# Optimization experiments

Measured on AMD Instinct MI355X. Metric: run time of the kernel, lower is better.

The kernel has to match this reference:

```python
import jax, jax.numpy as jnp
import numpy as np
import math

HEADS = 16
ROPE_BASE = 10000.0


def _alibi_slopes(n):
    # power-of-2 branch of ALiBiBias._get_slopes (n=16 is a power of 2)
    start = 2.0 ** (-(2.0 ** (-(math.log2(n) - 3))))
    return np.array([start * (start ** i) for i in range(n)], dtype=np.float32)


def _rope_cos_sin(T, head_dim):
    # RotaryPositionalEmbedding: inv_freq over even indices, emb = cat(freqs, freqs)
    inv_freq = 1.0 / (ROPE_BASE ** (jnp.arange(0, head_dim, 2, dtype=jnp.float32) / head_dim))
    t = jnp.arange(T, dtype=jnp.float32)
    f = t[:, None] * inv_freq[None, :]            # (T, head_dim//2)
    emb = jnp.concatenate([f, f], axis=-1)        # (T, head_dim)
    # apply_rotary_pos_emb takes cos/sin of emb then strides [0::2]
    cos = jnp.cos(emb)[:, 0::2]                   # (T, head_dim//2)
    sin = jnp.sin(emb)[:, 0::2]
    return cos, sin


def _apply_rope(x, cos, sin):
    # x: (B,H,T,hd); cos/sin: (T, hd//2)
    x1 = x[..., 0::2]
    x2 = x[..., 1::2]
    r1 = x1 * cos - x2 * sin
    r2 = x2 * cos + x1 * sin
    # interleave back: out[...,0::2]=r1, out[...,1::2]=r2
    return jnp.stack([r1, r2], axis=-1).reshape(x.shape)


def setup_inputs() -> dict:
    key = jax.random.key(0)
    k1, k2, k3, k4 = jax.random.split(key, 4)
    B, T, C = 2, 2048, 1024
    x = jax.random.normal(k1, (B, T, C), dtype=jnp.float32)
    W_qkv = jax.random.normal(k2, (C, 3 * C), dtype=jnp.float32) * 0.02
    W_out = jax.random.normal(k3, (C, C), dtype=jnp.float32) * 0.02
    b_out = jax.random.normal(k4, (C,), dtype=jnp.float32) * 0.02
    return {"x": x, "W_qkv": W_qkv, "W_out": W_out, "b_out": b_out}


def reference(x, W_qkv, W_out, b_out):
    B, T, C = x.shape
    H = HEADS
    hd = C // H

    qkv = (x @ W_qkv).reshape(B, T, 3, H, hd)
    qkv = jnp.transpose(qkv, (2, 0, 3, 1, 4))     # (3, B, H, T, hd)
    q, k, v = qkv[0], qkv[1], qkv[2]

    cos, sin = _rope_cos_sin(T, hd)
    q = _apply_rope(q, cos, sin)
    k = _apply_rope(k, cos, sin)

    scores = jnp.einsum('bhqd,bhkd->bhqk', q, k) / jnp.sqrt(jnp.float32(hd))

    # ALiBi bias: -slope_h * |i - j|
    slopes = jnp.asarray(_alibi_slopes(H))        # (H,)
    pos = jnp.arange(T, dtype=jnp.float32)
    dist = jnp.abs(pos[None, :] - pos[:, None])   # (T, T)
    scores = scores - slopes[None, :, None, None] * dist[None, None, :, :]

    attn = jax.nn.softmax(scores, axis=-1)
    out = jnp.einsum('bhqk,bhkd->bhqd', attn, v)  # (B,H,T,hd)
    out = jnp.transpose(out, (0, 2, 1, 3)).reshape(B, T, C)
    out = out @ W_out + b_out
    return out, attn
```

## Files before the change

### kernel.cpp

```cpp
#include <hip/hip_runtime.h>
#include <hip/hip_bf16.h>

typedef __bf16 bf16_t;
typedef __bf16 bf16x8 __attribute__((ext_vector_type(8)));
typedef __bf16 bf16x4 __attribute__((ext_vector_type(4)));
typedef float floatx4 __attribute__((ext_vector_type(4)));

#define NB 2
#define NT 2048
#define NC 1024
#define NH 16
#define HD 64
#define BT (NB*NT)

#define GLL16(g, l) __builtin_amdgcn_global_load_lds( \
    (const __attribute__((address_space(1))) void*)(g), \
    (__attribute__((address_space(3))) void*)(l), 16, 0, 0)

__global__ void k_cvt_x(const float* __restrict__ x, bf16_t* __restrict__ xb, int n){
  int i = (blockIdx.x*blockDim.x + threadIdx.x)*4;
  if (i >= n) return;
  float4 v = *(const float4*)(x+i);
  bf16_t o[4] = {(bf16_t)v.x,(bf16_t)v.y,(bf16_t)v.z,(bf16_t)v.w};
  *(uint2*)(xb+i) = *(const uint2*)o;
}

__global__ void k_cvt_t(const float* __restrict__ in, bf16_t* __restrict__ out, int K, int N){
  __shared__ float tile[32][33];
  int tid = threadIdx.x;
  int kt = blockIdx.y*32, nt = blockIdx.x*32;
  int row = tid>>3, c4 = (tid&7)*4;
  float4 v = *(const float4*)(in + (size_t)(kt+row)*N + nt + c4);
  tile[row][c4+0]=v.x; tile[row][c4+1]=v.y; tile[row][c4+2]=v.z; tile[row][c4+3]=v.w;
  __syncthreads();
  bf16_t o[4];
  #pragma unroll
  for (int i=0;i<4;i++) o[i] = (bf16_t)tile[c4+i][row];
  *(uint2*)(out + (size_t)(nt+row)*K + kt + c4) = *(const uint2*)o;
}

__global__ void k_trv(const bf16_t* __restrict__ qkv, bf16_t* __restrict__ Vt){
  __shared__ float tile[32][33];
  int tid = threadIdx.x;
  int bh = blockIdx.z; int b = bh>>4, h = bh&15;
  int t0 = blockIdx.y*32, d0 = blockIdx.x*32;
  int row = tid>>3, c4 = (tid&7)*4;
  bf16x4 v = *(const bf16x4*)(qkv + (size_t)(b*NT + t0 + row)*3072 + 2048 + h*HD + d0 + c4);
  #pragma unroll
  for (int i=0;i<4;i++) tile[row][c4+i] = (float)v[i];
  __syncthreads();
  bf16x4 o;
  #pragma unroll
  for (int i=0;i<4;i++) o[i] = (bf16_t)tile[c4+i][row];
  *(bf16x4*)(Vt + ((size_t)bh*HD + d0 + row)*NT + t0 + c4) = o;
}

template<int MI, bool BIAS, bool OUTBF>
__global__ __launch_bounds__(256) void k_gemm(
    const bf16_t* __restrict__ A, const bf16_t* __restrict__ Bt,
    void* __restrict__ Cv, const float* __restrict__ bias, int M, int N, int K){
  constexpr int BM = MI*32;
  __shared__ __align__(16) bf16_t As[BM][64];
  __shared__ __align__(16) bf16_t Bs[128][64];
  int tid = threadIdx.x;
  int wave = tid>>6, lane = tid&63, quad = lane>>4, l15 = lane&15;
  int m0 = blockIdx.y*BM, n0 = blockIdx.x*128;
  int wm = (wave>>1)*(MI*16), wn = (wave&1)*64;
  floatx4 acc[MI][4];
  #pragma unroll
  for(int i=0;i<MI;i++)
    #pragma unroll
    for(int j=0;j<4;j++) acc[i][j] = (floatx4){0.f,0.f,0.f,0.f};
  int srow = lane>>3;
  int sslot = (lane&7) ^ srow;
  const bf16_t* Ag = A  + (size_t)(m0 + wave*(MI*8) + srow)*K + sslot*8;
  const bf16_t* Bg = Bt + (size_t)(n0 + wave*32 + srow)*K + sslot*8;
  int rs = l15 & 7;
  for (int k0=0; k0<K; k0+=64){
    #pragma unroll
    for (int i=0;i<MI;i++)
      GLL16(Ag + (size_t)(i*8)*K + k0, &As[wave*(MI*8) + i*8][0]);
    #pragma unroll
    for (int i=0;i<4;i++)
      GLL16(Bg + (size_t)(i*8)*K + k0, &Bs[wave*32 + i*8][0]);
    __syncthreads();
    bf16x8 af[2][MI], bfr[2][4];
    #pragma unroll
    for (int kk=0;kk<2;kk++){
      #pragma unroll
      for (int mi=0;mi<MI;mi++) af[kk][mi]  = *(const bf16x8*)&As[wm+mi*16+l15][8*((kk*4+quad) ^ rs)];
      #pragma unroll
      for (int ni=0;ni<4;ni++)  bfr[kk][ni] = *(const bf16x8*)&Bs[wn+ni*16+l15][8*((kk*4+quad) ^ rs)];
    }
    #pragma unroll
    for (int kk=0;kk<2;kk++)
      #pragma unroll
      for (int mi=0;mi<MI;mi++)
        #pragma unroll
        for (int ni=0;ni<4;ni++)
          acc[mi][ni] = __builtin_amdgcn_mfma_f32_16x16x32_bf16(af[kk][mi], bfr[kk][ni], acc[mi][ni],0,0,0);
    __syncthreads();
  }
  #pragma unroll
  for (int ni=0;ni<4;ni++){
    int col = n0 + wn + ni*16 + l15;
    float bv = 0.f; if (BIAS) bv = bias[col];
    #pragma unroll
    for (int mi=0;mi<MI;mi++){
      int rowb = m0 + wm + mi*16 + quad*4;
      #pragma unroll
      for (int r=0;r<4;r++){
        float v = acc[mi][ni][r] + bv;
        if (OUTBF) ((bf16_t*)Cv)[(size_t)(rowb+r)*N + col] = (bf16_t)v;
        else       ((float*)Cv)[(size_t)(rowb+r)*N + col]  = v;
      }
    }
  }
}

__global__ void k_rope(const bf16_t* __restrict__ qkv, bf16_t* __restrict__ Qb,
                       bf16_t* __restrict__ Kb){
  int p = blockIdx.x*blockDim.x + threadIdx.x;
  int r = p >> 10;
  int c = (p & 1023)*2;
  int s = c >> 10, rem = c & 1023;
  int h = rem >> 6, d = rem & 63, j = d >> 1;
  int b = r >> 11, t = r & 2047;
  float x1 = (float)qkv[(size_t)r*3072 + c];
  float x2 = (float)qkv[(size_t)r*3072 + c + 1];
  float freq = exp2f(-0.8304820237218406f * (float)(j & 15));
  float ang = (float)t * freq;
  float sn, cs;
  __sincosf(ang, &sn, &cs);
  float o1 = x1*cs - x2*sn;
  float o2 = x2*cs + x1*sn;
  bf16_t* dst = (s==0) ? Qb : Kb;
  bf16_t o[2] = {(bf16_t)o1, (bf16_t)o2};
  *(unsigned int*)(dst + (size_t)((b*NH + h)*NT + t)*HD + d) = *(const unsigned int*)o;
}

__global__ __launch_bounds__(512) void k_attn(
    const bf16_t* __restrict__ Qb, const bf16_t* __restrict__ Kb, const bf16_t* __restrict__ Vtg,
    float* __restrict__ attn, bf16_t* __restrict__ Ob){
  __shared__ __align__(16) bf16_t Ks[64][64];
  __shared__ __align__(16) bf16_t Vs[64][64];
  __shared__ __align__(16) bf16_t Ps[8][16][64];
  int tid = threadIdx.x;
  int wave = tid>>6, lane = tid&63, quad = lane>>4, l15 = lane&15;
  int qt = blockIdx.x, bh = blockIdx.y;
  int h = bh & (NH-1);
  const float LOG2E = 1.4426950408889634f;
  float slope2 = exp2f(-0.5f*(float)(h+1)) * LOG2E;
  const float c1 = 0.125f * LOG2E;
  int qbase = qt*128 + wave*16;
  const bf16_t* qrow = Qb + ((size_t)bh*NT + qbase + l15)*HD;
  bf16x8 qa0 = *(const bf16x8*)(qrow + quad*8);
  bf16x8 qa1 = *(const bf16x8*)(qrow + 32 + quad*8);
  int srow = lane>>3, sslot = (lane&7) ^ srow;
  const bf16_t* kg = Kb  + ((size_t)bh*NT + wave*8 + srow)*HD + sslot*8;
  const bf16_t* vg = Vtg + ((size_t)bh*HD + wave*8 + srow)*NT + sslot*8;
  const floatx4 z4 = {0.f,0.f,0.f,0.f};
  int rs = l15 & 7;

  float lsum[4] = {0.f,0.f,0.f,0.f};
  for (int k0=0;k0<NT;k0+=64){
    GLL16(kg + (size_t)k0*HD, &Ks[wave*8][0]);
    __syncthreads();
    #pragma unroll
    for (int nt=0;nt<4;nt++){
      bf16x8 kb0 = *(const bf16x8*)&Ks[nt*16+l15][8*((quad)   ^ rs)];
      bf16x8 kb1 = *(const bf16x8*)&Ks[nt*16+l15][8*((4+quad) ^ rs)];
      floatx4 sv = __builtin_amdgcn_mfma_f32_16x16x32_bf16(qa0, kb0, z4,0,0,0);
      sv = __builtin_amdgcn_mfma_f32_16x16x32_bf16(qa1, kb1, sv,0,0,0);
      float fk = (float)(qbase + quad*4 - (k0 + nt*16 + l15));
      #pragma unroll
      for (int r=0;r<4;r++){
        float arg = fmaf(sv[r], c1, -slope2*fabsf(fk + (float)r));
        lsum[r] += exp2f(arg);
      }
    }
    __syncthreads();
  }
  #pragma unroll
  for (int r=0;r<4;r++){
    #pragma unroll
    for (int off=1;off<16;off<<=1) lsum[r] += __shfl_xor(lsum[r], off, 16);
  }
  float invl[4];
  #pragma unroll
  for (int r=0;r<4;r++) invl[r] = 1.f / lsum[r];

  floatx4 oacc[4] = {z4,z4,z4,z4};
  float* attnrow = attn + (size_t)bh*NT*NT;
  for (int k0=0;k0<NT;k0+=64){
    GLL16(kg + (size_t)k0*HD, &Ks[wave*8][0]);
    GLL16(vg + k0,            &Vs[wave*8][0]);
    __syncthreads();
    #pragma unroll
    for (int nt=0;nt<4;nt++){
      bf16x8 kb0 = *(const bf16x8*)&Ks[nt*16+l15][8*((quad)   ^ rs)];
      bf16x8 kb1 = *(const bf16x8*)&Ks[nt*16+l15][8*((4+quad) ^ rs)];
      floatx4 sv = __builtin_amdgcn_mfma_f32_16x16x32_bf16(qa0, kb0, z4,0,0,0);
      sv = __builtin_amdgcn_mfma_f32_16x16x32_bf16(qa1, kb1, sv,0,0,0);
      int kpos = k0 + nt*16 + l15;
      float fk = (float)(qbase + quad*4 - kpos);
      #pragma unroll
      for (int r=0;r<4;r++){
        float arg = fmaf(sv[r], c1, -slope2*fabsf(fk + (float)r));
        float pv = exp2f(arg) * invl[r];
        int qpos = qbase + quad*4 + r;
        __builtin_nontemporal_store(pv, &attnrow[(size_t)qpos*NT + kpos]);
        Ps[wave][quad*4+r][ 8*(((nt*2) + (l15>>3)) ^ ((quad*4+r)&7)) + (l15&7) ] = (bf16_t)pv;
      }
    }
    #pragma unroll
    for (int ks=0;ks<2;ks++){
      bf16x8 pa = *(const bf16x8*)&Ps[wave][l15][8*((ks*4+quad) ^ rs)];
      #pragma unroll
      for (int dt=0;dt<4;dt++){
        bf16x8 vb = *(const bf16x8*)&Vs[dt*16+l15][8*((ks*4+quad) ^ rs)];
        oacc[dt] = __builtin_amdgcn_mfma_f32_16x16x32_bf16(pa, vb, oacc[dt],0,0,0);
      }
    }
    __syncthreads();
  }
  int b = bh >> 4;
  #pragma unroll
  for (int dt=0;dt<4;dt++){
    #pragma unroll
    for (int r=0;r<4;r++){
      int t = qbase + quad*4 + r;
      Ob[(size_t)(b*NT + t)*NC + h*HD + dt*16 + l15] = (bf16_t)oacc[dt][r];
    }
  }
}

extern "C" void kernel_launch(void* const* d_in, const int* in_sizes, int n_in,
                              void* d_out, int out_size, void* d_ws, size_t ws_size,
                              hipStream_t stream){
  const float* x    = (const float*)d_in[0];
  const float* Wqkv = (const float*)d_in[1];
  const float* Wout = (const float*)d_in[2];
  const float* bout = (const float*)d_in[3];
  (void)in_sizes; (void)n_in; (void)out_size; (void)ws_size;

  char* ws = (char*)d_ws;
  size_t off = 0;
  auto alloc = [&](size_t elems)->bf16_t* {
    bf16_t* p = (bf16_t*)(ws + off);
    off += ((elems*sizeof(bf16_t) + 255)/256)*256;
    return p;
  };
  bf16_t* Xb   = alloc((size_t)BT*NC);
  bf16_t* Wqt  = alloc((size_t)3*NC*NC);
  bf16_t* Wot  = alloc((size_t)NC*NC);
  bf16_t* QKVb = alloc((size_t)BT*3*NC);
  bf16_t* Qb   = alloc((size_t)NB*NH*NT*HD);
  bf16_t* Kb   = alloc((size_t)NB*NH*NT*HD);
  bf16_t* Vtg  = alloc((size_t)NB*NH*HD*NT);
  bf16_t* Ob   = alloc((size_t)BT*NC);

  k_cvt_x<<<(BT*NC/4)/256, 256, 0, stream>>>(x, Xb, BT*NC);
  k_cvt_t<<<dim3(3*NC/32, NC/32), 256, 0, stream>>>(Wqkv, Wqt, NC, 3*NC);
  k_cvt_t<<<dim3(NC/32,   NC/32), 256, 0, stream>>>(Wout, Wot, NC, NC);
  k_gemm<4,false,true><<<dim3(3*NC/128, BT/128), 256, 0, stream>>>(Xb, Wqt, (void*)QKVb, nullptr, BT, 3*NC, NC);
  k_rope<<<(BT*1024)/256, 256, 0, stream>>>(QKVb, Qb, Kb);
  k_trv<<<dim3(HD/32, NT/32, NB*NH), 256, 0, stream>>>(QKVb, Vtg);
  float* attn = (float*)d_out + (size_t)BT*NC;
  k_attn<<<dim3(NT/128, NB*NH), 512, 0, stream>>>(Qb, Kb, Vtg, attn, Ob);
  k_gemm<2,true,false><<<dim3(NC/128, BT/64), 256, 0, stream>>>(Ob, Wot, d_out, bout, BT, NC, NC);
}
```

Measured before the change: 758.7 us.

## Transpose score MFMA, drop LDS staging of K/V, vectorize attention-prob stores

The attention kernel now computes S^T by swapping MFMA operands (K as A, Q as B), so each lane owns one query row and four consecutive keys. That lets each lane write four attention probabilities as one 16-byte nontemporal store instead of scalar strided stores. K and V are read straight from global/L2 rather than staged through LDS, which removes every __syncthreads. Blocks shrink to 256 threads over 64 queries, and normalisation is folded into the exponent via -log2(sum). The risk is that K/V are re-read from global per wave with no LDS reuse, which raises L2 traffic.

```diff
diff --git a/kernel.cpp b/kernel.cpp
--- a/kernel.cpp
+++ b/kernel.cpp
@@ -139,12 +139,10 @@
   *(unsigned int*)(dst + (size_t)((b*NH + h)*NT + t)*HD + d) = *(const unsigned int*)o;
 }
 
-__global__ __launch_bounds__(512) void k_attn(
+__global__ __launch_bounds__(256) void k_attn(
     const bf16_t* __restrict__ Qb, const bf16_t* __restrict__ Kb, const bf16_t* __restrict__ Vtg,
     float* __restrict__ attn, bf16_t* __restrict__ Ob){
-  __shared__ __align__(16) bf16_t Ks[64][64];
-  __shared__ __align__(16) bf16_t Vs[64][64];
-  __shared__ __align__(16) bf16_t Ps[8][16][64];
+  __shared__ __align__(16) bf16_t Ps[4][16][64];
   int tid = threadIdx.x;
   int wave = tid>>6, lane = tid&63, quad = lane>>4, l15 = lane&15;
   int qt = blockIdx.x, bh = blockIdx.y;
@@ -152,77 +150,71 @@
   const float LOG2E = 1.4426950408889634f;
   float slope2 = exp2f(-0.5f*(float)(h+1)) * LOG2E;
   const float c1 = 0.125f * LOG2E;
-  int qbase = qt*128 + wave*16;
-  const bf16_t* qrow = Qb + ((size_t)bh*NT + qbase + l15)*HD;
+  int qbase = qt*64 + wave*16;
+  int qpos = qbase + l15;
+  const bf16_t* qrow = Qb + ((size_t)bh*NT + qpos)*HD;
   bf16x8 qa0 = *(const bf16x8*)(qrow + quad*8);
   bf16x8 qa1 = *(const bf16x8*)(qrow + 32 + quad*8);
-  int srow = lane>>3, sslot = (lane&7) ^ srow;
-  const bf16_t* kg = Kb  + ((size_t)bh*NT + wave*8 + srow)*HD + sslot*8;
-  const bf16_t* vg = Vtg + ((size_t)bh*HD + wave*8 + srow)*NT + sslot*8;
+  const bf16_t* kg = Kb  + (size_t)bh*NT*HD;
+  const bf16_t* vg = Vtg + (size_t)bh*HD*NT;
   const floatx4 z4 = {0.f,0.f,0.f,0.f};
   int rs = l15 & 7;
-
-  float lsum[4] = {0.f,0.f,0.f,0.f};
+  char* psrow = (char*)&Ps[wave][l15][0];
+
+  float lsum = 0.f;
   for (int k0=0;k0<NT;k0+=64){
-    GLL16(kg + (size_t)k0*HD, &Ks[wave*8][0]);
-    __syncthreads();
     #pragma unroll
     for (int nt=0;nt<4;nt++){
-      bf16x8 kb0 = *(const bf16x8*)&Ks[nt*16+l15][8*((quad)   ^ rs)];
-      bf16x8 kb1 = *(const bf16x8*)&Ks[nt*16+l15][8*((4+quad) ^ rs)];
-      floatx4 sv = __builtin_amdgcn_mfma_f32_16x16x32_bf16(qa0, kb0, z4,0,0,0);
-      sv = __builtin_amdgcn_mfma_f32_16x16x32_bf16(qa1, kb1, sv,0,0,0);
-      float fk = (float)(qbase + quad*4 - (k0 + nt*16 + l15));
+      const bf16_t* kr = kg + (size_t)(k0+nt*16+l15)*HD + quad*8;
+      bf16x8 ka0 = *(const bf16x8*)(kr);
+      bf16x8 ka1 = *(const bf16x8*)(kr + 32);
+      floatx4 sv = __builtin_amdgcn_mfma_f32_16x16x32_bf16(ka0, qa0, z4,0,0,0);
+      sv = __builtin_amdgcn_mfma_f32_16x16x32_bf16(ka1, qa1, sv,0,0,0);
+      float fk = (float)(qpos - (k0 + nt*16 + quad*4));
       #pragma unroll
       for (int r=0;r<4;r++){
-        float arg = fmaf(sv[r], c1, -slope2*fabsf(fk + (float)r));
-        lsum[r] += exp2f(arg);
-      }
-    }
-    __syncthreads();
-  }
-  #pragma unroll
-  for (int r=0;r<4;r++){
-    #pragma unroll
-    for (int off=1;off<16;off<<=1) lsum[r] += __shfl_xor(lsum[r], off, 16);
-  }
-  float invl[4];
-  #pragma unroll
-  for (int r=0;r<4;r++) invl[r] = 1.f / lsum[r];
+        float arg = fmaf(sv[r], c1, -slope2*fabsf(fk - (float)r));
+        lsum += exp2f(arg);
+      }
+    }
+  }
+  lsum += __shfl_xor(lsum, 16);
+  lsum += __shfl_xor(lsum, 32);
+  float li = -__log2f(lsum);
 
   floatx4 oacc[4] = {z4,z4,z4,z4};
-  float* attnrow = attn + (size_t)bh*NT*NT;
+  float* attnrow = attn + (size_t)bh*NT*NT + (size_t)qpos*NT;
   for (int k0=0;k0<NT;k0+=64){
-    GLL16(kg + (size_t)k0*HD, &Ks[wave*8][0]);
-    GLL16(vg + k0,            &Vs[wave*8][0]);
-    __syncthreads();
     #pragma unroll
     for (int nt=0;nt<4;nt++){
-      bf16x8 kb0 = *(const bf16x8*)&Ks[nt*16+l15][8*((quad)   ^ rs)];
-      bf16x8 kb1 = *(const bf16x8*)&Ks[nt*16+l15][8*((4+quad) ^ rs)];
-      floatx4 sv = __builtin_amdgcn_mfma_f32_16x16x32_bf16(qa0, kb0, z4,0,0,0);
-      sv = __builtin_amdgcn_mfma_f32_16x16x32_bf16(qa1, kb1, sv,0,0,0);
-      int kpos = k0 + nt*16 + l15;
-      float fk = (float)(qbase + quad*4 - kpos);
+      const bf16_t* kr = kg + (size_t)(k0+nt*16+l15)*HD + quad*8;
+      bf16x8 ka0 = *(const bf16x8*)(kr);
+      bf16x8 ka1 = *(const bf16x8*)(kr + 32);
+      floatx4 sv = __builtin_amdgcn_mfma_f32_16x16x32_bf16(ka0, qa0, z4,0,0,0);
+      sv = __builtin_amdgcn_mfma_f32_16x16x32_bf16(ka1, qa1, sv,0,0,0);
+      float fk = (float)(qpos - (k0 + nt*16 + quad*4));
+      float p[4];
       #pragma unroll
       for (int r=0;r<4;r++){
-        float arg = fmaf(sv[r], c1, -slope2*fabsf(fk + (float)r));
-        float pv = exp2f(arg) * invl[r];
-        int qpos = qbase + quad*4 + r;
-        __builtin_nontemporal_store(pv, &attnrow[(size_t)qpos*NT + kpos]);
-        Ps[wave][quad*4+r][ 8*(((nt*2) + (l15>>3)) ^ ((quad*4+r)&7)) + (l15&7) ] = (bf16_t)pv;
-      }
+        float arg = fmaf(sv[r], c1, fmaf(-slope2, fabsf(fk - (float)r), li));
+        p[r] = exp2f(arg);
+      }
+      floatx4 st = {p[0],p[1],p[2],p[3]};
+      __builtin_nontemporal_store(st, (floatx4*)(attnrow + k0 + nt*16 + quad*4));
+      bf16x4 pb;
+      #pragma unroll
+      for (int r=0;r<4;r++) pb[r] = (bf16_t)p[r];
+      *(bf16x4*)(psrow + (((nt*2 + (quad>>1)) ^ rs)*16 + (quad&1)*8)) = pb;
     }
     #pragma unroll
     for (int ks=0;ks<2;ks++){
-      bf16x8 pa = *(const bf16x8*)&Ps[wave][l15][8*((ks*4+quad) ^ rs)];
+      bf16x8 pa = *(const bf16x8*)(psrow + ((ks*4+quad) ^ rs)*16);
       #pragma unroll
       for (int dt=0;dt<4;dt++){
-        bf16x8 vb = *(const bf16x8*)&Vs[dt*16+l15][8*((ks*4+quad) ^ rs)];
+        bf16x8 vb = *(const bf16x8*)(vg + (size_t)(dt*16+l15)*NT + k0 + ks*32 + quad*8);
         oacc[dt] = __builtin_amdgcn_mfma_f32_16x16x32_bf16(pa, vb, oacc[dt],0,0,0);
       }
     }
-    __syncthreads();
   }
   int b = bh >> 4;
   #pragma unroll
@@ -267,6 +259,6 @@
   k_rope<<<(BT*1024)/256, 256, 0, stream>>>(QKVb, Qb, Kb);
   k_trv<<<dim3(HD/32, NT/32, NB*NH), 256, 0, stream>>>(QKVb, Vtg);
   float* attn = (float*)d_out + (size_t)BT*NC;
-  k_attn<<<dim3(NT/128, NB*NH), 512, 0, stream>>>(Qb, Kb, Vtg, attn, Ob);
+  k_attn<<<dim3(NT/64, NB*NH), 256, 0, stream>>>(Qb, Kb, Vtg, attn, Ob);
   k_gemm<2,true,false><<<dim3(NC/128, BT/64), 256, 0, stream>>>(Ob, Wot, d_out, bout, BT, NC, NC);
 }
```

Result: slower. 912.0 us (+20.2%).
